# Kernel tuning notes

Measured on AMD Instinct MI355X. Metric: run time of the kernel, lower is better.

## Reference

```python
import jax, jax.numpy as jnp
import numpy as np

DIM = 1024
NUM_HEADS = 16
HEAD_DIM = DIM // NUM_HEADS


def setup_inputs() -> dict:
    key = jax.random.key(0)
    ks = jax.random.split(key, 9)
    s = 1.0 / np.sqrt(DIM)
    x = jax.random.normal(ks[0], (2, 2048, DIM), dtype=jnp.float32)
    Wq = jax.random.normal(ks[1], (DIM, DIM), dtype=jnp.float32) * s
    bq = jax.random.normal(ks[2], (DIM,), dtype=jnp.float32) * s
    Wk = jax.random.normal(ks[3], (DIM, DIM), dtype=jnp.float32) * s
    bk = jax.random.normal(ks[4], (DIM,), dtype=jnp.float32) * s
    Wv = jax.random.normal(ks[5], (DIM, DIM), dtype=jnp.float32) * s
    bv = jax.random.normal(ks[6], (DIM,), dtype=jnp.float32) * s
    Wo = jax.random.normal(ks[7], (DIM, DIM), dtype=jnp.float32) * s
    bo = jax.random.normal(ks[8], (DIM,), dtype=jnp.float32) * s
    return {"x": x, "Wq": Wq, "bq": bq, "Wk": Wk, "bk": bk,
            "Wv": Wv, "bv": bv, "Wo": Wo, "bo": bo}


def _softmax_one(x, axis=-1):
    # softmax with +1 in the denominator (quiet attention)
    x = x - jnp.max(x, axis=axis, keepdims=True)
    ex = jnp.exp(x)
    return ex / (1.0 + jnp.sum(ex, axis=axis, keepdims=True))


def reference(x, Wq, bq, Wk, bk, Wv, bv, Wo, bo):
    B, L, D = x.shape
    H, hd = NUM_HEADS, HEAD_DIM
    q = (x @ Wq + bq).reshape(B, L, H, hd).transpose(0, 2, 1, 3)  # b h l d
    k = (x @ Wk + bk).reshape(B, L, H, hd).transpose(0, 2, 1, 3)
    v = (x @ Wv + bv).reshape(B, L, H, hd).transpose(0, 2, 1, 3)
    scores = jnp.einsum('bhqd,bhkd->bhqk', q, k) / np.sqrt(hd).astype(np.float32)
    # causal additive mask: -inf above the diagonal (matches torch generate_square_subsequent_mask)
    causal = jnp.triu(jnp.full((L, L), -jnp.inf, dtype=scores.dtype), k=1)
    scores = scores + causal
    attn = _softmax_one(scores, axis=-1)
    ctx = jnp.einsum('bhqk,bhkd->bhqd', attn, v)
    ctx = ctx.transpose(0, 2, 1, 3).reshape(B, L, D)
    return ctx @ Wo + bo
```

## Files before the change

### kernel.cpp

```cpp
#include <hip/hip_runtime.h>
#include <hip/hip_bf16.h>
#include <cstdint>
#include <cstddef>

#define DIMN 1024
#define NHEAD 16
#define HDIM 64
#define NB 2
#define SEQ 2048
#define MROWS 4096
#define BHN 32
#define QKV_STRIDE 4194304
#define BH_ELEMS 131072

#define QSCALE 0.18033688011112042f

typedef float f32x4 __attribute__((ext_vector_type(4)));
typedef __bf16 bf16x8 __attribute__((ext_vector_type(8)));

__device__ __forceinline__ void async_copy16(const void* g, void* l) {
    __builtin_amdgcn_global_load_lds(
        (__attribute__((address_space(1))) void*)(g),
        (__attribute__((address_space(3))) void*)(l), 16, 0, 0);
}

__device__ __forceinline__ unsigned short bf16_bits(float f) {
    __hip_bfloat16 hb = __float2bfloat16(f);
    return *(unsigned short*)&hb;
}

__device__ __forceinline__ float fast_exp2(float x) {
    return __builtin_amdgcn_exp2f(x);
}

__global__ __launch_bounds__(256) void prep_kernel(
        const float* __restrict__ x, const float* __restrict__ bq,
        const float* __restrict__ bk, const float* __restrict__ bv,
        const float* __restrict__ Wq, const float* __restrict__ Wk,
        const float* __restrict__ Wv, const float* __restrict__ Wo,
        __hip_bfloat16* __restrict__ xbf, float* __restrict__ biasq,
        __hip_bfloat16* __restrict__ wqkvt, __hip_bfloat16* __restrict__ wot) {
    __shared__ float tile[32][33];
    const int bid = blockIdx.x;
    const int t = threadIdx.x;
    if (bid < 4096) {
        int i = (bid * 256 + t) * 4;
        float4 v = *(const float4*)(x + i);
        xbf[i + 0] = __float2bfloat16(v.x);
        xbf[i + 1] = __float2bfloat16(v.y);
        xbf[i + 2] = __float2bfloat16(v.z);
        xbf[i + 3] = __float2bfloat16(v.w);
    } else if (bid < 4099) {
        int base = (bid - 4096) * 1024 + t * 4;
#pragma unroll
        for (int e = 0; e < 4; e++) {
            int gi = base + e;
            int which = gi >> 10, off = gi & 1023;
            float v = (which == 0) ? bq[off] : (which == 1) ? bk[off] : bv[off];
            biasq[gi] = v;
        }
    } else {
        int rr = bid - 4099;
        int z = rr >> 10;
        int tid = rr & 1023;
        int n0 = (tid & 31) * 32, k0 = (tid >> 5) * 32;
        const float* in = (z == 0) ? Wq : (z == 1) ? Wk : (z == 2) ? Wv : Wo;
        __hip_bfloat16* out = (z == 3) ? wot : wqkvt + (size_t)z * DIMN * DIMN;
        int tx = t & 31, ty = t >> 5;
#pragma unroll
        for (int r = 0; r < 32; r += 8)
            tile[ty + r][tx] = in[(size_t)(k0 + ty + r) * DIMN + n0 + tx];
        __syncthreads();
#pragma unroll
        for (int r = 0; r < 32; r += 8)
            out[(size_t)(n0 + ty + r) * DIMN + k0 + tx] =
                __float2bfloat16(tile[tx][ty + r]);
    }
}

__global__ __launch_bounds__(512, 1) void gemm_qkv_kernel(
        const __hip_bfloat16* __restrict__ A, const __hip_bfloat16* __restrict__ Bt,
        const float* __restrict__ bias, __hip_bfloat16* __restrict__ qkv,
        __hip_bfloat16* __restrict__ vt) {
    __shared__ __align__(16) unsigned short SM[49152];
    const int t = threadIdx.x;
    const int m0 = blockIdx.y * 256;
    const int n0 = blockIdx.x * 256;
    const int lane = t & 63;
    const int w = t >> 6;
    const int wmid = w >> 2;
    const int wnid = w & 3;
    const int r16 = lane & 15;
    const int quad = lane >> 4;
    const int rsw = (quad ^ ((r16 >> 1) & 3)) * 8;
    const int blr0 = (wnid & 1) * 64;

    const int srow = t >> 2;
    const int scsw = (t & 3) ^ ((srow >> 1) & 3);
    const __hip_bfloat16* Ag = A + (size_t)(m0 + srow) * DIMN + scsw * 8;
    const __hip_bfloat16* Bg = Bt + (size_t)(n0 + srow) * DIMN + scsw * 8;

    f32x4 acc[8][4];
#pragma unroll
    for (int i = 0; i < 8; i++)
#pragma unroll
        for (int j = 0; j < 4; j++) acc[i][j] = (f32x4){0.f, 0.f, 0.f, 0.f};

#pragma unroll
    for (int tt = 0; tt < 2; tt++) {
#pragma unroll
        for (int h = 0; h < 2; h++)
            async_copy16(Ag + (size_t)h * 131072 + tt * 32,
                         (char*)(SM + (tt * 2 + h) * 4096 + t * 8));
#pragma unroll
        for (int h = 0; h < 2; h++)
            async_copy16(Bg + (size_t)h * 131072 + tt * 32,
                         (char*)(SM + 24576 + (tt * 2 + h) * 4096 + t * 8));
    }

    int sl = 0;
#pragma unroll 1
    for (int tt = 0; tt < 32; ++tt) {
        const int sl2 = (sl >= 1) ? (sl - 1) : 2;
        if (tt == 31) {
            asm volatile("s_waitcnt vmcnt(0)" ::: "memory");
        } else {
            asm volatile("s_waitcnt vmcnt(4)" ::: "memory");
        }
        __builtin_amdgcn_s_barrier();

        const unsigned short* Asl = SM + (sl * 2 + wmid) * 4096;
        const unsigned short* Bsl = SM + 24576 + (sl * 2 + (wnid >> 1)) * 4096;

        bf16x8 af[8], bfr[4];
#pragma unroll
        for (int i = 0; i < 8; i++)
            af[i] = *(const bf16x8*)&Asl[(i * 16 + r16) * 32 + rsw];
#pragma unroll
        for (int j = 0; j < 4; j++)
            bfr[j] = *(const bf16x8*)&Bsl[(blr0 + j * 16 + r16) * 32 + rsw];

        if (tt < 30) {
#pragma unroll
            for (int h = 0; h < 2; h++) {
                async_copy16(Ag + (size_t)h * 131072 + (tt + 2) * 32,
                             (char*)(SM + (sl2 * 2 + h) * 4096 + t * 8));
                async_copy16(Bg + (size_t)h * 131072 + (tt + 2) * 32,
                             (char*)(SM + 24576 + (sl2 * 2 + h) * 4096 + t * 8));
            }
        }

        __builtin_amdgcn_s_setprio(1);
#pragma unroll
        for (int i = 0; i < 8; i++)
#pragma unroll
            for (int j = 0; j < 4; j++)
                acc[i][j] = __builtin_amdgcn_mfma_f32_16x16x32_bf16(
                    af[i], bfr[j], acc[i][j], 0, 0, 0);
        __builtin_amdgcn_s_setprio(0);

        sl = (sl < 2) ? (sl + 1) : 0;
    }

    const int which = n0 >> 10;
#pragma unroll
    for (int j = 0; j < 4; j++) {
        const int n = n0 + wnid * 64 + j * 16 + r16;
        const float bv = bias[n];
        const int rem = n & 1023;
        const int h = rem >> 6, d = rem & 63;
#pragma unroll
        for (int i = 0; i < 8; i++) {
            const int mbase = m0 + wmid * 128 + i * 16 + quad * 4;
            const int b = mbase >> 11;
            const int lrow = mbase & 2047;
            const int bh = b * NHEAD + h;
            if (which == 2) {
                ushort4 pk;
                pk.x = bf16_bits(acc[i][j][0] + bv);
                pk.y = bf16_bits(acc[i][j][1] + bv);
                pk.z = bf16_bits(acc[i][j][2] + bv);
                pk.w = bf16_bits(acc[i][j][3] + bv);
                *(ushort4*)(vt + (size_t)bh * BH_ELEMS + (size_t)d * SEQ + lrow) = pk;
            } else {
#pragma unroll
                for (int r = 0; r < 4; r++) {
                    float v = acc[i][j][r] + bv;
                    if (which == 0) v *= QSCALE;
                    qkv[(size_t)which * QKV_STRIDE + (size_t)bh * BH_ELEMS +
                        (size_t)(lrow + r) * 64 + d] = __float2bfloat16(v);
                }
            }
        }
    }
}

__global__ __launch_bounds__(256) void gemm_out_kernel(
        const __hip_bfloat16* __restrict__ A, const __hip_bfloat16* __restrict__ Bt,
        const float* __restrict__ bias, float* __restrict__ outp) {
    __shared__ __align__(16) unsigned short As[64 * 32];
    __shared__ __align__(16) unsigned short Bs[128 * 32];
    const int t = threadIdx.x;
    const int m0 = blockIdx.y * 64;
    const int n0 = blockIdx.x * 128;
    const int lane = t & 63;
    const int w = t >> 6;
    const int wm = (w >> 1) * 32;
    const int wn = (w & 1) * 64;
    const int r16 = lane & 15;
    const int quad = lane >> 4;

    f32x4 acc[2][4];
#pragma unroll
    for (int i = 0; i < 2; i++)
#pragma unroll
        for (int j = 0; j < 4; j++) acc[i][j] = (f32x4){0.f, 0.f, 0.f, 0.f};

    const int rowA = t >> 2;
    const int kch = (t & 3) * 8;

    for (int k0 = 0; k0 < DIMN; k0 += 32) {
        __syncthreads();
        async_copy16(A + (size_t)(m0 + rowA) * DIMN + k0 + kch, (char*)As + t * 16);
#pragma unroll
        for (int r = 0; r < 2; r++) {
            int row = rowA + r * 64;
            async_copy16(Bt + (size_t)(n0 + row) * DIMN + k0 + kch,
                         (char*)Bs + (size_t)(row * 4 + (t & 3)) * 16);
        }
        __syncthreads();

        bf16x8 af[2], bfr[4];
#pragma unroll
        for (int i = 0; i < 2; i++)
            af[i] = *(const bf16x8*)&As[(wm + i * 16 + r16) * 32 + quad * 8];
#pragma unroll
        for (int j = 0; j < 4; j++)
            bfr[j] = *(const bf16x8*)&Bs[(wn + j * 16 + r16) * 32 + quad * 8];
#pragma unroll
        for (int i = 0; i < 2; i++)
#pragma unroll
            for (int j = 0; j < 4; j++)
                acc[i][j] = __builtin_amdgcn_mfma_f32_16x16x32_bf16(
                    af[i], bfr[j], acc[i][j], 0, 0, 0);
    }

#pragma unroll
    for (int i = 0; i < 2; i++)
#pragma unroll
        for (int j = 0; j < 4; j++) {
            int n = n0 + wn + j * 16 + r16;
            float bv = bias[n];
#pragma unroll
            for (int r = 0; r < 4; r++) {
                int m = m0 + wm + i * 16 + quad * 4 + r;
                outp[(size_t)m * DIMN + n] = acc[i][j][r] + bv;
            }
        }
}

__global__ __launch_bounds__(512, 4) void attn_mfma_kernel(
        const __hip_bfloat16* __restrict__ qkv, const __hip_bfloat16* __restrict__ vt,
        __hip_bfloat16* __restrict__ ctxout) {
    __shared__ __align__(16) unsigned short SMEM[36864];

    const int bx = blockIdx.x;
    const int g = bx >> 5;
    const int qt = (g < 8) ? 15 - g : g - 8;
    const int bh = bx & 31;
    const int t = threadIdx.x;
    const int lane = t & 63;
    const int w = t >> 6;
    const int half = w >> 2;
    const int wq = w & 3;
    const int r16 = lane & 15;
    const int quad = lane >> 4;
    const int qbase = qt * 128 + wq * 32;
    const int swz = quad ^ ((r16 >> 1) & 3);
    const int pkey = (r16 >> 1) & 3;

    const __hip_bfloat16* Qg = qkv + (size_t)bh * BH_ELEMS;
    const __hip_bfloat16* Kg = qkv + (size_t)QKV_STRIDE + (size_t)bh * BH_ELEMS;
    const __hip_bfloat16* Vtg = vt + (size_t)bh * BH_ELEMS;

    unsigned short* PsW = SMEM + 32768 + w * 512;

    const int cb_kp = (t & 511) >> 8;
    const int cb_rr = ((t & 511) >> 2) & 63;
    const int cb_cg = ((t & 511) & 3) ^ ((cb_rr >> 1) & 3);

    bf16x8 bq[2][2];
#pragma unroll
    for (int ng = 0; ng < 2; ng++)
#pragma unroll
        for (int kp = 0; kp < 2; kp++)
            bq[ng][kp] = *(const bf16x8*)(Qg + (size_t)(qbase + ng * 16 + r16) * 64 +
                                          kp * 32 + quad * 8);

    f32x4 oT[4][2];
#pragma unroll
    for (int mt = 0; mt < 4; mt++)
#pragma unroll
        for (int ng = 0; ng < 2; ng++) oT[mt][ng] = (f32x4){0.f, 0.f, 0.f, 0.f};
    float m_run[2] = {-1e30f, -1e30f};
    float z_run[2] = {0.f, 0.f};

    const int niter = qt + 1;

#pragma unroll
    for (int it = 0; it < 2; it++) {
        int cl = it * 512 + t;
        int ktile = (cl >> 9) ? (qt + 1) : 0;
        async_copy16(Kg + (size_t)(ktile * 64 + cb_rr) * 64 + cb_kp * 32 + cb_cg * 8,
                     (char*)SMEM + (size_t)cl * 16);
        async_copy16(Vtg + (size_t)cb_rr * SEQ + ktile * 64 + cb_kp * 32 + cb_cg * 8,
                     (char*)SMEM + 32768 + (size_t)cl * 16);
    }

#pragma unroll 1
    for (int i = 0; i < niter; i++) {
        const int curb = i & 1;
        __syncthreads();

        if (i + 1 < niter) {
            int ktA = i + 1;
            int ktB = qt + 2 + i; if (ktB > 31) ktB = 31;
#pragma unroll
            for (int it = 0; it < 2; it++) {
                int cl = it * 512 + t;
                int ktile = (cl >> 9) ? ktB : ktA;
                async_copy16(Kg + (size_t)(ktile * 64 + cb_rr) * 64 + cb_kp * 32 + cb_cg * 8,
                             (char*)SMEM + (size_t)(curb ^ 1) * 16384 + (size_t)cl * 16);
                async_copy16(Vtg + (size_t)cb_rr * SEQ + ktile * 64 + cb_kp * 32 + cb_cg * 8,
                             (char*)SMEM + 32768 + (size_t)(curb ^ 1) * 16384 + (size_t)cl * 16);
            }
        }

        const int ktile = half ? (qt + 1 + i) : i;
        const bool active = (ktile * 64 <= qbase + 31);

        if (active) {
            const unsigned short* KsW = SMEM + curb * 8192 + half * 4096;
            f32x4 st[4][2];
#pragma unroll
            for (int mt = 0; mt < 4; mt++)
#pragma unroll
                for (int ng = 0; ng < 2; ng++) st[mt][ng] = (f32x4){0.f, 0.f, 0.f, 0.f};
#pragma unroll
            for (int mt = 0; mt < 4; mt++)
#pragma unroll
                for (int kp = 0; kp < 2; kp++) {
                    bf16x8 ak = *(const bf16x8*)&KsW[kp * 2048 + (mt * 16 + r16) * 32 + swz * 8];
                    st[mt][0] = __builtin_amdgcn_mfma_f32_16x16x32_bf16(ak, bq[0][kp], st[mt][0], 0, 0, 0);
                    st[mt][1] = __builtin_amdgcn_mfma_f32_16x16x32_bf16(ak, bq[1][kp], st[mt][1], 0, 0, 0);
                }

            if (ktile * 64 + 63 > qbase) {
#pragma unroll
                for (int mt = 0; mt < 4; mt++) {
                    int kb = ktile * 64 + mt * 16 + quad * 4;
#pragma unroll
                    for (int ng = 0; ng < 2; ng++) {
                        int q = qbase + ng * 16 + r16;
#pragma unroll
                        for (int r = 0; r < 4; r++)
                            if (kb + r > q) st[mt][ng][r] = -__builtin_inff();
                    }
                }
            }

#pragma unroll
            for (int mt = 0; mt < 4; mt++)
#pragma unroll
                for (int ng = 0; ng < 2; ng++) {
                    float s0 = st[mt][ng][0], s1 = st[mt][ng][1];
                    float s2 = st[mt][ng][2], s3 = st[mt][ng][3];
                    m_run[ng] = fmaxf(m_run[ng], fmaxf(fmaxf(s0, s1), fmaxf(s2, s3)));
                    float p0 = fast_exp2(s0), p1 = fast_exp2(s1);
                    float p2 = fast_exp2(s2), p3 = fast_exp2(s3);
                    z_run[ng] += (p0 + p1) + (p2 + p3);
                    st[mt][ng][0] = p0; st[mt][ng][1] = p1;
                    st[mt][ng][2] = p2; st[mt][ng][3] = p3;
                }

            const unsigned short* VsW = SMEM + 16384 + curb * 8192 + half * 4096;
#pragma unroll
            for (int p = 0; p < 2; p++) {
#pragma unroll
                for (int ng = 0; ng < 2; ng++) {
#pragma unroll
                    for (int ml = 0; ml < 2; ml++) {
                        int mt = p * 2 + ml;
                        ushort4 pk;
                        pk.x = bf16_bits(st[mt][ng][0]);
                        pk.y = bf16_bits(st[mt][ng][1]);
                        pk.z = bf16_bits(st[mt][ng][2]);
                        pk.w = bf16_bits(st[mt][ng][3]);
                        int c = (ml * 2 + (quad >> 1)) ^ pkey;
                        *(ushort4*)&PsW[r16 * 32 + c * 8 + (quad & 1) * 4] = pk;
                    }
                    bf16x8 bp = *(const bf16x8*)&PsW[r16 * 32 + (quad ^ pkey) * 8];
#pragma unroll
                    for (int mt = 0; mt < 4; mt++) {
                        bf16x8 av = *(const bf16x8*)&VsW[p * 2048 + (mt * 16 + r16) * 32 + swz * 8];
                        oT[mt][ng] = __builtin_amdgcn_mfma_f32_16x16x32_bf16(
                            av, bp, oT[mt][ng], 0, 0, 0);
                    }
                }
            }
        }
    }

#pragma unroll
    for (int off = 16; off < 64; off <<= 1)
#pragma unroll
        for (int ng = 0; ng < 2; ng++) {
            m_run[ng] = fmaxf(m_run[ng], __shfl_xor(m_run[ng], off, 64));
            z_run[ng] += __shfl_xor(z_run[ng], off, 64);
        }

    __syncthreads();
    f32x4* CbO = (f32x4*)SMEM;
    f32x4* Ml = (f32x4*)((char*)SMEM + 32768);
    if (w >= 4) {
        int w4 = w - 4;
#pragma unroll
        for (int mt = 0; mt < 4; mt++)
#pragma unroll
            for (int ng = 0; ng < 2; ng++)
                CbO[((w4 * 8 + mt * 2 + ng) << 6) + lane] = oT[mt][ng];
        f32x4 ml;
        ml[0] = m_run[0]; ml[1] = m_run[1]; ml[2] = z_run[0]; ml[3] = z_run[1];
        Ml[(w4 << 6) + lane] = ml;
    }
    __syncthreads();
    if (w < 4) {
        f32x4 ml = Ml[(w << 6) + lane];
        float rd[2];
#pragma unroll
        for (int ng = 0; ng < 2; ng++) {
            float mtot = fmaxf(m_run[ng], ml[ng]);
            float ztot = z_run[ng] + ml[2 + ng];
            rd[ng] = 1.f / (fast_exp2(mtot) + ztot);
        }
        const int b = bh >> 4, h = bh & 15;
#pragma unroll
        for (int mt = 0; mt < 4; mt++)
#pragma unroll
            for (int ng = 0; ng < 2; ng++) {
                f32x4 O1 = CbO[((w * 8 + mt * 2 + ng) << 6) + lane];
                int q = qbase + ng * 16 + r16;
                ushort4 pk;
                pk.x = bf16_bits((oT[mt][ng][0] + O1[0]) * rd[ng]);
                pk.y = bf16_bits((oT[mt][ng][1] + O1[1]) * rd[ng]);
                pk.z = bf16_bits((oT[mt][ng][2] + O1[2]) * rd[ng]);
                pk.w = bf16_bits((oT[mt][ng][3] + O1[3]) * rd[ng]);
                *(ushort4*)(ctxout + ((size_t)(b * SEQ + q)) * DIMN + h * 64 +
                            mt * 16 + quad * 4) = pk;
            }
    }
}


extern "C" void kernel_launch(void* const* d_in, const int* in_sizes, int n_in,
                              void* d_out, int out_size, void* d_ws, size_t ws_size,
                              hipStream_t stream) {
    const float* x  = (const float*)d_in[0];
    const float* Wq = (const float*)d_in[1];
    const float* bq = (const float*)d_in[2];
    const float* Wk = (const float*)d_in[3];
    const float* bk = (const float*)d_in[4];
    const float* Wv = (const float*)d_in[5];
    const float* bv = (const float*)d_in[6];
    const float* Wo = (const float*)d_in[7];
    const float* bo = (const float*)d_in[8];

    char* ws = (char*)d_ws;
    __hip_bfloat16* xbf   = (__hip_bfloat16*)(ws);
    __hip_bfloat16* wqkvt = (__hip_bfloat16*)(ws + (8u << 20));
    __hip_bfloat16* wot   = (__hip_bfloat16*)(ws + (14u << 20));
    float*          biasq = (float*)(ws + (16u << 20));
    __hip_bfloat16* qkv   = (__hip_bfloat16*)(ws + (16u << 20) + 65536u);
    __hip_bfloat16* vt    = (__hip_bfloat16*)(ws + (16u << 20) + 65536u + (16u << 20));
    __hip_bfloat16* ctx   = (__hip_bfloat16*)(ws + (16u << 20) + 65536u + (24u << 20));
    float* out = (float*)d_out;

    prep_kernel<<<8195, 256, 0, stream>>>(x, bq, bk, bv, Wq, Wk, Wv, Wo,
                                          xbf, biasq, wqkvt, wot);
    gemm_qkv_kernel<<<dim3(12, 16), 512, 0, stream>>>(xbf, wqkvt, biasq, qkv, vt);
    attn_mfma_kernel<<<512, 512, 0, stream>>>(qkv, vt, ctx);
    gemm_out_kernel<<<dim3(8, 64), 256, 0, stream>>>(ctx, wot, bo, out);
}
```

Baseline: 176.9 us.

## Retile QKV GEMM to 256x192 so the grid fills all compute units

Shrinks the QKV projection GEMM tile width from 256 to 192 columns, raising the grid from 192 to 256 blocks so every CU on the device gets a block. Each warp now covers 48 columns (3 MFMA tiles), and the B-tile load is split so that half the threads load the extra 64 rows. Wait counts are adjusted per warp. The trade-off is lower arithmetic intensity per block and uneven load issue across warps.

```diff
diff --git a/kernel.cpp b/kernel.cpp
--- a/kernel.cpp
+++ b/kernel.cpp
@@ -82,10 +82,10 @@
         const __hip_bfloat16* __restrict__ A, const __hip_bfloat16* __restrict__ Bt,
         const float* __restrict__ bias, __hip_bfloat16* __restrict__ qkv,
         __hip_bfloat16* __restrict__ vt) {
-    __shared__ __align__(16) unsigned short SM[49152];
+    __shared__ __align__(16) unsigned short SM[43008];
     const int t = threadIdx.x;
     const int m0 = blockIdx.y * 256;
-    const int n0 = blockIdx.x * 256;
+    const int n0 = blockIdx.x * 192;
     const int lane = t & 63;
     const int w = t >> 6;
     const int wmid = w >> 2;
@@ -93,18 +93,19 @@
     const int r16 = lane & 15;
     const int quad = lane >> 4;
     const int rsw = (quad ^ ((r16 >> 1) & 3)) * 8;
-    const int blr0 = (wnid & 1) * 64;
+    const bool bstage2 = (w < 4);
 
     const int srow = t >> 2;
     const int scsw = (t & 3) ^ ((srow >> 1) & 3);
-    const __hip_bfloat16* Ag = A + (size_t)(m0 + srow) * DIMN + scsw * 8;
-    const __hip_bfloat16* Bg = Bt + (size_t)(n0 + srow) * DIMN + scsw * 8;
-
-    f32x4 acc[8][4];
+    const __hip_bfloat16* Ag  = A  + (size_t)(m0 + srow) * DIMN + scsw * 8;
+    const __hip_bfloat16* Bg1 = Bt + (size_t)(n0 + srow) * DIMN + scsw * 8;
+    const __hip_bfloat16* Bg2 = Bt + (size_t)(n0 + 128 + srow) * DIMN + scsw * 8;
+
+    f32x4 acc[8][3];
 #pragma unroll
     for (int i = 0; i < 8; i++)
 #pragma unroll
-        for (int j = 0; j < 4; j++) acc[i][j] = (f32x4){0.f, 0.f, 0.f, 0.f};
+        for (int j = 0; j < 3; j++) acc[i][j] = (f32x4){0.f, 0.f, 0.f, 0.f};
 
 #pragma unroll
     for (int tt = 0; tt < 2; tt++) {
@@ -112,10 +113,10 @@
         for (int h = 0; h < 2; h++)
             async_copy16(Ag + (size_t)h * 131072 + tt * 32,
                          (char*)(SM + (tt * 2 + h) * 4096 + t * 8));
-#pragma unroll
-        for (int h = 0; h < 2; h++)
-            async_copy16(Bg + (size_t)h * 131072 + tt * 32,
-                         (char*)(SM + 24576 + (tt * 2 + h) * 4096 + t * 8));
+        async_copy16(Bg1 + tt * 32, (char*)(SM + 24576 + tt * 6144 + t * 8));
+        if (bstage2)
+            async_copy16(Bg2 + tt * 32,
+                         (char*)(SM + 24576 + tt * 6144 + 4096 + t * 8));
     }
 
     int sl = 0;
@@ -124,37 +125,41 @@
         const int sl2 = (sl >= 1) ? (sl - 1) : 2;
         if (tt == 31) {
             asm volatile("s_waitcnt vmcnt(0)" ::: "memory");
+        } else if (bstage2) {
+            asm volatile("s_waitcnt vmcnt(4)" ::: "memory");
         } else {
-            asm volatile("s_waitcnt vmcnt(4)" ::: "memory");
+            asm volatile("s_waitcnt vmcnt(3)" ::: "memory");
         }
         __builtin_amdgcn_s_barrier();
 
         const unsigned short* Asl = SM + (sl * 2 + wmid) * 4096;
-        const unsigned short* Bsl = SM + 24576 + (sl * 2 + (wnid >> 1)) * 4096;
-
-        bf16x8 af[8], bfr[4];
+        const unsigned short* Bsl = SM + 24576 + sl * 6144;
+
+        bf16x8 af[8], bfr[3];
 #pragma unroll
         for (int i = 0; i < 8; i++)
             af[i] = *(const bf16x8*)&Asl[(i * 16 + r16) * 32 + rsw];
 #pragma unroll
-        for (int j = 0; j < 4; j++)
-            bfr[j] = *(const bf16x8*)&Bsl[(blr0 + j * 16 + r16) * 32 + rsw];
+        for (int j = 0; j < 3; j++)
+            bfr[j] = *(const bf16x8*)&Bsl[(wnid * 48 + j * 16 + r16) * 32 + rsw];
 
         if (tt < 30) {
 #pragma unroll
-            for (int h = 0; h < 2; h++) {
+            for (int h = 0; h < 2; h++)
                 async_copy16(Ag + (size_t)h * 131072 + (tt + 2) * 32,
                              (char*)(SM + (sl2 * 2 + h) * 4096 + t * 8));
-                async_copy16(Bg + (size_t)h * 131072 + (tt + 2) * 32,
-                             (char*)(SM + 24576 + (sl2 * 2 + h) * 4096 + t * 8));
-            }
+            async_copy16(Bg1 + (tt + 2) * 32,
+                         (char*)(SM + 24576 + sl2 * 6144 + t * 8));
+            if (bstage2)
+                async_copy16(Bg2 + (tt + 2) * 32,
+                             (char*)(SM + 24576 + sl2 * 6144 + 4096 + t * 8));
         }
 
         __builtin_amdgcn_s_setprio(1);
 #pragma unroll
         for (int i = 0; i < 8; i++)
 #pragma unroll
-            for (int j = 0; j < 4; j++)
+            for (int j = 0; j < 3; j++)
                 acc[i][j] = __builtin_amdgcn_mfma_f32_16x16x32_bf16(
                     af[i], bfr[j], acc[i][j], 0, 0, 0);
         __builtin_amdgcn_s_setprio(0);
@@ -162,19 +167,20 @@
         sl = (sl < 2) ? (sl + 1) : 0;
     }
 
-    const int which = n0 >> 10;
-#pragma unroll
-    for (int j = 0; j < 4; j++) {
-        const int n = n0 + wnid * 64 + j * 16 + r16;
+#pragma unroll
+    for (int j = 0; j < 3; j++) {
+        const int nb = n0 + wnid * 48 + j * 16;
+        const int n = nb + r16;
         const float bv = bias[n];
+        const int which = nb >> 10;
         const int rem = n & 1023;
-        const int h = rem >> 6, d = rem & 63;
+        const int hh = rem >> 6, d = rem & 63;
 #pragma unroll
         for (int i = 0; i < 8; i++) {
             const int mbase = m0 + wmid * 128 + i * 16 + quad * 4;
             const int b = mbase >> 11;
             const int lrow = mbase & 2047;
-            const int bh = b * NHEAD + h;
+            const int bh = b * NHEAD + hh;
             if (which == 2) {
                 ushort4 pk;
                 pk.x = bf16_bits(acc[i][j][0] + bv);
@@ -487,7 +493,7 @@
 
     prep_kernel<<<8195, 256, 0, stream>>>(x, bq, bk, bv, Wq, Wk, Wv, Wo,
                                           xbf, biasq, wqkvt, wot);
-    gemm_qkv_kernel<<<dim3(12, 16), 512, 0, stream>>>(xbf, wqkvt, biasq, qkv, vt);
+    gemm_qkv_kernel<<<dim3(16, 16), 512, 0, stream>>>(xbf, wqkvt, biasq, qkv, vt);
     attn_mfma_kernel<<<512, 512, 0, stream>>>(qkv, vt, ctx);
     gemm_out_kernel<<<dim3(8, 64), 256, 0, stream>>>(ctx, wot, bo, out);
 }
```

New measurement: 172.4 us. -2.6%, faster.
